# Kernel optimization log

Measured on AMD Instinct MI355X. Metric: run time of the kernel, lower is better.

The kernel has to match this reference:

```python
import jax, jax.numpy as jnp
import numpy as np

LN_EPS = 1e-5  # torch.nn.LayerNorm default

def g(x):
    # minGRU activation: x + 0.5 for x >= 0, sigmoid(x) otherwise (always positive)
    return jnp.where(x >= 0, x + 0.5, jax.nn.sigmoid(x))

def log_g(x):
    return jnp.where(x >= 0, jnp.log(jax.nn.relu(x) + 0.5), -jax.nn.softplus(-x))

def layernorm(x, gamma, beta):
    mu = jnp.mean(x, axis=-1, keepdims=True)
    var = jnp.var(x, axis=-1, keepdims=True)
    return (x - mu) * jax.lax.rsqrt(var + LN_EPS) * gamma + beta

def mingru_scan(gate, hidden, h0):
    # gate, hidden: (B,S,D); h0: (B,1,D) positive
    # z = sigmoid(gate); h_t = (1-z_t)*h_{t-1} + z_t * g(hidden_t)
    # evaluated via Heinsen parallel scan in log space
    log_z = -jax.nn.softplus(-gate)          # log sigmoid(gate)
    log_coeffs = -jax.nn.softplus(gate)      # log(1 - sigmoid(gate))
    log_h0 = jnp.log(h0)                     # (B,1,D)
    log_tilde_h = log_g(hidden)
    a_star = jnp.cumsum(
        jnp.concatenate([jnp.zeros_like(log_h0), log_coeffs], axis=1), axis=1
    )                                        # (B,S+1,D)
    log_vals = jnp.concatenate([log_h0, log_z + log_tilde_h], axis=1) - a_star
    log_h = a_star + jax.lax.cumlogsumexp(log_vals, axis=1)
    return jnp.exp(log_h)[:, 1:]             # (B,S,D)

def setup_inputs() -> dict:
    key = jax.random.key(0)
    k1, k2 = jax.random.split(key)
    B, S, D, L = 8, 4096, 1024, 3
    x = jax.random.normal(k1, (B, S, D), dtype=jnp.float32)
    W = jax.random.normal(k2, (L, D, 2 * D), dtype=jnp.float32) * 0.02
    b = jnp.zeros((L, 2 * D), dtype=jnp.float32)
    ln_gamma = jnp.ones((L, D), dtype=jnp.float32)
    ln_beta = jnp.zeros((L, D), dtype=jnp.float32)
    return {"x": x, "ln_gamma": ln_gamma, "ln_beta": ln_beta, "W": W, "b": b}

def reference(x, ln_gamma, ln_beta, W, b):
    B, S, D = x.shape
    L = W.shape[0]
    inp = x
    next_hidden = []
    for l in range(L):
        h_prev = jnp.full((B, 1, D), 0.5, dtype=x.dtype)  # g(zeros) = 0.5
        xn = layernorm(inp, ln_gamma[l], ln_beta[l])
        gh = jnp.einsum('bsd,de->bse', xn, W[l]) + b[l]   # (B,S,2D)
        gate, hidden = jnp.split(gh, 2, axis=2)
        out = mingru_scan(gate, hidden, h_prev)
        next_hidden.append(out[:, -1:])
        out = out + inp  # residual (sizes equal -> identity res_align)
        inp = out
    return (out, *next_hidden)
```

## Files before the change

kernel.cpp:

```cpp
#include <hip/hip_runtime.h>

typedef unsigned short u16;
typedef unsigned int   u32;
typedef float  f32x2  __attribute__((ext_vector_type(2)));
typedef float  f32x4  __attribute__((ext_vector_type(4)));
typedef short  bf16x8 __attribute__((ext_vector_type(8)));
typedef u16    u16x4  __attribute__((ext_vector_type(4)));
typedef u32    u32x4  __attribute__((ext_vector_type(4)));

#define BQ 8
#define SQ 4096
#define DQ 1024
#define NQ 2048
#define MQ 32768
#define KQ 1024
#define CCH 128
#define TCH 32
#define NT 16

__device__ __forceinline__ float bf2f(u16 u){
  union { u32 i; float f; } v; v.i = ((u32)u) << 16; return v.f;
}
__device__ __forceinline__ u16 f2bf(float f){
  union { float f; u32 i; } v; v.f = f;
  u32 r = v.i + 0x7fffu + ((v.i >> 16) & 1u);
  return (u16)(r >> 16);
}

__device__ __forceinline__ void sig_ab(float gate, float hid, float& a, float& bv){
  float eg = __expf(gate);
  float a_ = __builtin_amdgcn_rcpf(1.f + eg);
  float z  = 1.f - a_;
  float eh = __expf(hid);
  float sg = eh * __builtin_amdgcn_rcpf(1.f + eh);
  float gval = (hid >= 0.f) ? (hid + 0.5f) : sg;
  a = a_; bv = z * gval;
}

__device__ __forceinline__ void gload_lds16(const u16* g, u16* l){
  __builtin_amdgcn_global_load_lds(
      (const __attribute__((address_space(1))) u32*)g,
      (__attribute__((address_space(3)))       u32*)l,
      16, 0, 0);
}

__global__ __launch_bounds__(256) void wt_cast(const float* __restrict__ W,
                                               u16* __restrict__ WT){
  __shared__ float t[64][65];
  const int l  = blockIdx.z;
  const int k0 = blockIdx.x << 6, n0 = blockIdx.y << 6;
  const float* Wl = W  + (size_t)l * KQ * NQ;
  u16*         Tl = WT + (size_t)l * NQ * KQ;
  const int c = threadIdx.x & 63, r4 = threadIdx.x >> 6;
  #pragma unroll
  for (int i = 0; i < 16; ++i){
    int r = i * 4 + r4;
    t[r][c] = Wl[(size_t)(k0 + r) * NQ + n0 + c];
  }
  __syncthreads();
  #pragma unroll
  for (int i = 0; i < 16; ++i){
    int r = i * 4 + r4;
    Tl[(size_t)(n0 + r) * KQ + k0 + c] = f2bf(t[c][r]);
  }
}

__global__ __launch_bounds__(256) void ln_cast(const float* __restrict__ x,
                                               const float* __restrict__ gamma,
                                               const float* __restrict__ beta,
                                               u16* __restrict__ xn){
  const size_t row = blockIdx.x;
  const int tid = threadIdx.x;
  f32x4 xv = *(const f32x4*)(x + row * DQ + tid * 4);
  float s  = xv[0] + xv[1] + xv[2] + xv[3];
  float s2 = xv[0]*xv[0] + xv[1]*xv[1] + xv[2]*xv[2] + xv[3]*xv[3];
  #pragma unroll
  for (int off = 32; off > 0; off >>= 1){
    s  += __shfl_down(s,  off);
    s2 += __shfl_down(s2, off);
  }
  __shared__ float red[8];
  const int wave = tid >> 6, lane = tid & 63;
  if (lane == 0){ red[wave] = s; red[4 + wave] = s2; }
  __syncthreads();
  s  = red[0] + red[1] + red[2] + red[3];
  s2 = red[4] + red[5] + red[6] + red[7];
  const float mean = s * (1.f / DQ);
  float var = fmaxf(s2 * (1.f / DQ) - mean * mean, 0.f);
  const float rstd = rsqrtf(var + 1e-5f);
  f32x4 gv = *(const f32x4*)(gamma + tid * 4);
  f32x4 bv = *(const f32x4*)(beta  + tid * 4);
  u16x4 o;
  #pragma unroll
  for (int e = 0; e < 4; ++e) o[e] = f2bf((xv[e] - mean) * rstd * gv[e] + bv[e]);
  *(u16x4*)(xn + row * DQ + tid * 4) = o;
}

__global__ __launch_bounds__(512, 2) void gemm_k8(const u16* __restrict__ A,
                                                  const u16* __restrict__ Bt,
                                                  const float* __restrict__ bias,
                                                  u32* __restrict__ abv,
                                                  float* __restrict__ pq){
  __shared__ u16 lds[2][2][2][8192];
  const int bid = blockIdx.x;
  const int swz = ((bid & 7) << 7) | (bid >> 3);
  const int bn = swz & 7, bm = swz >> 3;
  const int m0 = bm << 8;
  const int tid = threadIdx.x;
  const int w = tid >> 6, lane = tid & 63;
  const int wr = w >> 2, wc = w & 3;
  const int lr = lane & 15, hi = lane >> 4;
  const int sl8 = lane >> 3;
  const int sslot = (lane & 7) ^ sl8;

  f32x4 acc[2][2][4][2] = {};
  bf16x8 afrA[4][2], afrB[4][2];
  bf16x8 bf0[2][2], bf1[2][2];

#define FENCE asm volatile("" ::: "memory")
#define BAR do { FENCE; __builtin_amdgcn_s_barrier(); FENCE; } while(0)

#define STAGE(op, hf, kt, pb_) do {                                            \
    const u16* gsrc_ = (op) ? Bt : A;                                          \
    const int rb_ = (op) ? ((bn << 7) + (hf) * 1024) : (m0 + ((hf) << 7));     \
    _Pragma("unroll")                                                          \
    for (int g_ = 0; g_ < 2; ++g_){                                            \
      const int row_ = (w << 4) + (g_ << 3) + sl8;                             \
      gload_lds16(gsrc_ + (size_t)(rb_ + row_) * KQ + ((kt) << 6) + (sslot << 3),\
                  &lds[pb_][op][hf][((w << 4) + (g_ << 3)) << 6]);             \
    }                                                                          \
  } while(0)

#define LDSRD(dst, base_, row_, slot_) do {                                    \
    const int r_ = (row_);                                                     \
    dst = *(const bf16x8*)((const char*)(base_) +                              \
          ((r_ << 7) + ((((slot_)) ^ (r_ & 7)) << 4)));                        \
  } while(0)

#define RD_A(dst, hf, buf_) do {                                               \
    const u16* Ah_ = &lds[buf_][0][hf][0];                                     \
    _Pragma("unroll")                                                          \
    for (int i_ = 0; i_ < 4; ++i_)                                             \
      _Pragma("unroll")                                                        \
      for (int kk_ = 0; kk_ < 2; ++kk_)                                        \
        LDSRD(dst[i_][kk_], Ah_, (wr << 6) + (i_ << 4) + lr, (kk_ << 2) + hi); \
  } while(0)

#define RD_B(dst, hf, buf_) do {                                               \
    const u16* Bh_ = &lds[buf_][1][hf][0];                                     \
    _Pragma("unroll")                                                          \
    for (int j_ = 0; j_ < 2; ++j_)                                             \
      _Pragma("unroll")                                                        \
      for (int kk_ = 0; kk_ < 2; ++kk_)                                        \
        LDSRD(dst[j_][kk_], Bh_, (wc << 5) + (j_ << 4) + lr, (kk_ << 2) + hi); \
  } while(0)

#define MM(qm, qn, AR, B) do {                                                 \
    _Pragma("unroll")                                                          \
    for (int kk_ = 0; kk_ < 2; ++kk_)                                          \
      _Pragma("unroll")                                                        \
      for (int i_ = 0; i_ < 4; ++i_)                                           \
        _Pragma("unroll")                                                      \
        for (int j_ = 0; j_ < 2; ++j_)                                         \
          acc[qm][qn][i_][j_] = __builtin_amdgcn_mfma_f32_16x16x32_bf16(       \
              AR[i_][kk_], B[j_][kk_], acc[qm][qn][i_][j_], 0, 0, 0);          \
  } while(0)

  STAGE(0, 0, 0, 0); STAGE(1, 0, 0, 0); STAGE(0, 1, 0, 0); STAGE(1, 1, 0, 0);

  for (int t = 0; t < NT; ++t){
    const int pb = t & 1, qb = pb ^ 1;
    const bool s = (t + 1 < NT);
    asm volatile("s_waitcnt vmcnt(0)" ::: "memory");
    BAR;
    if (s){
      STAGE(0, 0, t + 1, qb); STAGE(1, 0, t + 1, qb);
      STAGE(0, 1, t + 1, qb); STAGE(1, 1, t + 1, qb);
    }
    RD_A(afrA, 0, pb); RD_B(bf0, 0, pb);
    RD_A(afrB, 1, pb); RD_B(bf1, 1, pb);
    __builtin_amdgcn_s_setprio(1);
    MM(0, 0, afrA, bf0);
    MM(0, 1, afrA, bf1);
    MM(1, 0, afrB, bf0);
    MM(1, 1, afrB, bf1);
    __builtin_amdgcn_s_setprio(0);
  }
#undef MM
#undef RD_B
#undef RD_A
#undef LDSRD
#undef STAGE

  const int dbase = (bn << 7) + (wc << 5) + lr;
  #pragma unroll
  for (int qm = 0; qm < 2; ++qm){
    const int row00 = m0 + (qm << 7) + (wr << 6);
    #pragma unroll
    for (int half = 0; half < 2; ++half){
      float chP[2] = {1.f, 1.f}, chQ[2] = {0.f, 0.f};
      #pragma unroll
      for (int ii = 0; ii < 2; ++ii){
        const int i = (half << 1) + ii;
        float sgP[2] = {1.f, 1.f}, sgQ[2] = {0.f, 0.f};
        #pragma unroll
        for (int r = 0; r < 4; ++r){
          const int row = row00 + (i << 4) + (hi << 2) + r;
          #pragma unroll
          for (int j = 0; j < 2; ++j){
            const int d = dbase + (j << 4);
            float gate = acc[qm][0][i][j][r] + bias[d];
            float hid  = acc[qm][1][i][j][r] + bias[1024 + d];
            float a, bv; sig_ab(gate, hid, a, bv);
            u32 pk;
            asm volatile("v_cvt_pk_bf16_f32 %0, %1, %2"
                         : "=v"(pk) : "v"(a), "v"(bv));
            abv[(size_t)row * 1024 + d] = pk;
            union { u32 u; float f; } ua, ub;
            ua.u = pk << 16; ub.u = pk & 0xffff0000u;
            sgQ[j] = ua.f * sgQ[j] + ub.f;
            sgP[j] *= ua.f;
          }
        }
        #pragma unroll
        for (int j = 0; j < 2; ++j){
          float p = sgP[j], q = sgQ[j];
          float p1 = __shfl_up(p, 16), q1 = __shfl_up(q, 16);
          if (hi >= 1){ q = p * q1 + q; p = p * p1; }
          float p2 = __shfl_up(p, 32), q2 = __shfl_up(q, 32);
          if (hi >= 2){ q = p * q2 + q; p = p * p2; }
          chQ[j] = p * chQ[j] + q;
          chP[j] = p * chP[j];
        }
      }
      if (hi == 3){
        const int rowb = row00 + (half << 5);
        const int bq = rowb >> 12, cq = (rowb >> 5) & (CCH - 1);
        #pragma unroll
        for (int j = 0; j < 2; ++j){
          const int d = dbase + (j << 4);
          f32x2 v; v[0] = chP[j]; v[1] = chQ[j];
          *(f32x2*)(pq + ((((size_t)(bq * CCH + cq)) << 10) + d) * 2) = v;
        }
      }
    }
  }
#undef BAR
#undef FENCE
}

__global__ __launch_bounds__(256) void scan2(const float* __restrict__ pq,
                                             float* __restrict__ hst,
                                             float* __restrict__ hlast){
  const int idx = blockIdx.x * 256 + threadIdx.x;
  const int b = idx >> 10, d = idx & 1023;
  float h = 0.5f;
  for (int c = 0; c < CCH; ++c){
    const size_t o = ((size_t)(b * CCH + c) << 10) + d;
    hst[o] = h;
    f32x2 v = *(const f32x2*)(pq + o * 2);
    h = v[0] * h + v[1];
  }
  hlast[idx] = h;
}

template<int MODE>
__global__ __launch_bounds__(256) void scan3f(const u32* __restrict__ abv,
                                              const float* __restrict__ hst,
                                              const void* __restrict__ inp,
                                              void* __restrict__ outp,
                                              u16* __restrict__ xn,
                                              const float* __restrict__ gamma,
                                              const float* __restrict__ beta){
  const int b = blockIdx.x >> 7;
  const int c = blockIdx.x & (CCH - 1);
  const int tid = threadIdx.x;
  const int d4 = tid << 2;
  const int wave = tid >> 6, lane = tid & 63;
  const size_t srow = (size_t)b * SQ + (size_t)c * TCH;
  const u32* base = abv + srow * 1024 + d4;
  const size_t o = ((size_t)blockIdx.x << 10) + d4;
  f32x4 h0v = *(const f32x4*)(hst + o);
  float h[4] = {h0v[0], h0v[1], h0v[2], h0v[3]};
  __shared__ float red[2][8];
  f32x4 gv = {}, bvv = {};
  if (MODE != 2){
    gv  = *(const f32x4*)(gamma + d4);
    bvv = *(const f32x4*)(beta  + d4);
  }
  for (int t = 0; t < TCH; ++t){
    u32x4 ab = *(const u32x4*)(base + (size_t)t * 1024);
    f32x4 iv;
    if (MODE == 0){
      iv = *(const f32x4*)((const float*)inp + (srow + t) * DQ + d4);
    } else {
      u16x4 ib = *(const u16x4*)((const u16*)inp + (srow + t) * DQ + d4);
      #pragma unroll
      for (int e = 0; e < 4; ++e) iv[e] = bf2f(ib[e]);
    }
    f32x4 ov;
    #pragma unroll
    for (int e = 0; e < 4; ++e){
      const float a  = bf2f((u16)(ab[e] & 0xffffu));
      const float bv = bf2f((u16)(ab[e] >> 16));
      h[e] = a * h[e] + bv;
      ov[e] = h[e] + iv[e];
    }
    if (MODE == 2){
      *(f32x4*)((float*)outp + (srow + t) * DQ + d4) = ov;
    } else {
      u16x4 ob;
      #pragma unroll
      for (int e = 0; e < 4; ++e) ob[e] = f2bf(ov[e]);
      *(u16x4*)((u16*)outp + (srow + t) * DQ + d4) = ob;
      float s  = ov[0] + ov[1] + ov[2] + ov[3];
      float s2 = ov[0]*ov[0] + ov[1]*ov[1] + ov[2]*ov[2] + ov[3]*ov[3];
      #pragma unroll
      for (int off = 32; off > 0; off >>= 1){
        s  += __shfl_down(s,  off);
        s2 += __shfl_down(s2, off);
      }
      const int rb = t & 1;
      if (lane == 0){ red[rb][wave] = s; red[rb][4 + wave] = s2; }
      __syncthreads();
      s  = red[rb][0] + red[rb][1] + red[rb][2] + red[rb][3];
      s2 = red[rb][4] + red[rb][5] + red[rb][6] + red[rb][7];
      const float mean = s * (1.f / DQ);
      float var = fmaxf(s2 * (1.f / DQ) - mean * mean, 0.f);
      const float rstd = rsqrtf(var + 1e-5f);
      u16x4 xo;
      #pragma unroll
      for (int e = 0; e < 4; ++e)
        xo[e] = f2bf((ov[e] - mean) * rstd * gv[e] + bvv[e]);
      *(u16x4*)(xn + (srow + t) * DQ + d4) = xo;
    }
  }
}

extern "C" void kernel_launch(void* const* d_in, const int* in_sizes, int n_in,
                              void* d_out, int out_size, void* d_ws, size_t ws_size,
                              hipStream_t stream) {
  const float* x     = (const float*)d_in[0];
  const float* gamma = (const float*)d_in[1];
  const float* beta  = (const float*)d_in[2];
  const float* W     = (const float*)d_in[3];
  const float* bias  = (const float*)d_in[4];
  float* out = (float*)d_out;

  char* ws = (char*)d_ws;
  const size_t ACT = (size_t)MQ * DQ * 4;
  u16*   bufA = (u16*)(ws);
  u16*   bufB = (u16*)(ws + ACT);
  u32*   abv  = (u32*)(ws + 2 * ACT);
  u16*   xn   = (u16*)(ws + 3 * ACT);
  u16*   WT   = (u16*)(ws + 3 * ACT + (size_t)MQ * DQ * 2);
  float* pq   = (float*)(ws + 3 * ACT + (size_t)MQ * DQ * 2 + (size_t)3 * NQ * KQ * 2);
  float* hst  = pq + (size_t)2 * BQ * CCH * DQ;

  wt_cast<<<dim3(KQ / 64, NQ / 64, 3), 256, 0, stream>>>(W, WT);

  const dim3 ggrid((NQ / 256) * (MQ / 256));
  ln_cast<<<MQ, 256, 0, stream>>>(x, gamma, beta, xn);
  gemm_k8<<<ggrid, 512, 0, stream>>>(xn, WT, bias, abv, pq);
  scan2<<<(BQ * DQ) / 256, 256, 0, stream>>>(pq, hst, out + (size_t)MQ * DQ);
  scan3f<0><<<BQ * CCH, 256, 0, stream>>>(abv, hst, x, bufA, xn,
                                          gamma + DQ, beta + DQ);
  gemm_k8<<<ggrid, 512, 0, stream>>>(xn, WT + (size_t)NQ * KQ, bias + NQ,
                                     abv, pq);
  scan2<<<(BQ * DQ) / 256, 256, 0, stream>>>(pq, hst,
                                             out + (size_t)MQ * DQ + BQ * DQ);
  scan3f<1><<<BQ * CCH, 256, 0, stream>>>(abv, hst, bufA, bufB, xn,
                                          gamma + 2 * DQ, beta + 2 * DQ);
  gemm_k8<<<ggrid, 512, 0, stream>>>(xn, WT + (size_t)2 * NQ * KQ, bias + 2 * NQ,
                                     abv, pq);
  scan2<<<(BQ * DQ) / 256, 256, 0, stream>>>(pq, hst,
                                             out + (size_t)MQ * DQ + 2 * BQ * DQ);
  scan3f<2><<<BQ * CCH, 256, 0, stream>>>(abv, hst, bufB, out, nullptr,
                                          nullptr, nullptr);
}
```

Baseline: 720.5 us.

## Load GEMM B operand directly from global into registers, bypassing LDS

The B (weight) tile is no longer staged through shared memory. Each wave now reads its own B fragments straight from global memory into registers every k-step, while only A stays double-buffered in LDS. This halves LDS usage and removes the B LDS writes and reads. In exchange, the B loads are issued and consumed in the same iteration, so their global latency is not hidden behind the previous step. Waves in different rows also fetch the same B data redundantly.

```diff
diff --git a/kernel.cpp b/kernel.cpp
--- a/kernel.cpp
+++ b/kernel.cpp
@@ -101,7 +101,7 @@
                                                   const float* __restrict__ bias,
                                                   u32* __restrict__ abv,
                                                   float* __restrict__ pq){
-  __shared__ u16 lds[2][2][2][8192];
+  __shared__ u16 lds[2][2][8192];
   const int bid = blockIdx.x;
   const int swz = ((bid & 7) << 7) | (bid >> 3);
   const int bn = swz & 7, bm = swz >> 3;
@@ -112,23 +112,37 @@
   const int lr = lane & 15, hi = lane >> 4;
   const int sl8 = lane >> 3;
   const int sslot = (lane & 7) ^ sl8;
+  const int brow = (bn << 7) + (wc << 5) + lr;
 
   f32x4 acc[2][2][4][2] = {};
   bf16x8 afrA[4][2], afrB[4][2];
-  bf16x8 bf0[2][2], bf1[2][2];
+  bf16x8 bgl[2][2][2];
 
 #define FENCE asm volatile("" ::: "memory")
 #define BAR do { FENCE; __builtin_amdgcn_s_barrier(); FENCE; } while(0)
 
-#define STAGE(op, hf, kt, pb_) do {                                            \
-    const u16* gsrc_ = (op) ? Bt : A;                                          \
-    const int rb_ = (op) ? ((bn << 7) + (hf) * 1024) : (m0 + ((hf) << 7));     \
+#define STAGE_A(kt, pb_) do {                                                  \
     _Pragma("unroll")                                                          \
-    for (int g_ = 0; g_ < 2; ++g_){                                            \
-      const int row_ = (w << 4) + (g_ << 3) + sl8;                             \
-      gload_lds16(gsrc_ + (size_t)(rb_ + row_) * KQ + ((kt) << 6) + (sslot << 3),\
-                  &lds[pb_][op][hf][((w << 4) + (g_ << 3)) << 6]);             \
-    }                                                                          \
+    for (int hf_ = 0; hf_ < 2; ++hf_)                                          \
+      _Pragma("unroll")                                                        \
+      for (int g_ = 0; g_ < 2; ++g_){                                          \
+        const int row_ = (w << 4) + (g_ << 3) + sl8;                           \
+        gload_lds16(A + (size_t)(m0 + (hf_ << 7) + row_) * KQ + ((kt) << 6) +  \
+                        (sslot << 3),                                          \
+                    &lds[pb_][hf_][((w << 4) + (g_ << 3)) << 6]);              \
+      }                                                                        \
+  } while(0)
+
+#define LD_B(kt) do {                                                          \
+    _Pragma("unroll")                                                          \
+    for (int qn_ = 0; qn_ < 2; ++qn_)                                          \
+      _Pragma("unroll")                                                        \
+      for (int j_ = 0; j_ < 2; ++j_)                                           \
+        _Pragma("unroll")                                                      \
+        for (int kk_ = 0; kk_ < 2; ++kk_)                                      \
+          bgl[qn_][j_][kk_] = *(const bf16x8*)(Bt +                            \
+              ((size_t)(brow + qn_ * 1024 + (j_ << 4)) << 10) +                \
+              ((kt) << 6) + (kk_ << 5) + (hi << 3));                           \
   } while(0)
 
 #define LDSRD(dst, base_, row_, slot_) do {                                    \
@@ -138,7 +152,7 @@
   } while(0)
 
 #define RD_A(dst, hf, buf_) do {                                               \
-    const u16* Ah_ = &lds[buf_][0][hf][0];                                     \
+    const u16* Ah_ = &lds[buf_][hf][0];                                        \
     _Pragma("unroll")                                                          \
     for (int i_ = 0; i_ < 4; ++i_)                                             \
       _Pragma("unroll")                                                        \
@@ -146,16 +160,7 @@
         LDSRD(dst[i_][kk_], Ah_, (wr << 6) + (i_ << 4) + lr, (kk_ << 2) + hi); \
   } while(0)
 
-#define RD_B(dst, hf, buf_) do {                                               \
-    const u16* Bh_ = &lds[buf_][1][hf][0];                                     \
-    _Pragma("unroll")                                                          \
-    for (int j_ = 0; j_ < 2; ++j_)                                             \
-      _Pragma("unroll")                                                        \
-      for (int kk_ = 0; kk_ < 2; ++kk_)                                        \
-        LDSRD(dst[j_][kk_], Bh_, (wc << 5) + (j_ << 4) + lr, (kk_ << 2) + hi); \
-  } while(0)
-
-#define MM(qm, qn, AR, B) do {                                                 \
+#define MM(qm, qn, AR) do {                                                    \
     _Pragma("unroll")                                                          \
     for (int kk_ = 0; kk_ < 2; ++kk_)                                          \
       _Pragma("unroll")                                                        \
@@ -163,34 +168,31 @@
         _Pragma("unroll")                                                      \
         for (int j_ = 0; j_ < 2; ++j_)                                         \
           acc[qm][qn][i_][j_] = __builtin_amdgcn_mfma_f32_16x16x32_bf16(       \
-              AR[i_][kk_], B[j_][kk_], acc[qm][qn][i_][j_], 0, 0, 0);          \
-  } while(0)
-
-  STAGE(0, 0, 0, 0); STAGE(1, 0, 0, 0); STAGE(0, 1, 0, 0); STAGE(1, 1, 0, 0);
+              AR[i_][kk_], bgl[qn][j_][kk_], acc[qm][qn][i_][j_], 0, 0, 0);    \
+  } while(0)
+
+  STAGE_A(0, 0);
 
   for (int t = 0; t < NT; ++t){
     const int pb = t & 1, qb = pb ^ 1;
     const bool s = (t + 1 < NT);
     asm volatile("s_waitcnt vmcnt(0)" ::: "memory");
     BAR;
-    if (s){
-      STAGE(0, 0, t + 1, qb); STAGE(1, 0, t + 1, qb);
-      STAGE(0, 1, t + 1, qb); STAGE(1, 1, t + 1, qb);
-    }
-    RD_A(afrA, 0, pb); RD_B(bf0, 0, pb);
-    RD_A(afrB, 1, pb); RD_B(bf1, 1, pb);
+    if (s) STAGE_A(t + 1, qb);
+    LD_B(t);
+    RD_A(afrA, 0, pb); RD_A(afrB, 1, pb);
     __builtin_amdgcn_s_setprio(1);
-    MM(0, 0, afrA, bf0);
-    MM(0, 1, afrA, bf1);
-    MM(1, 0, afrB, bf0);
-    MM(1, 1, afrB, bf1);
+    MM(0, 0, afrA);
+    MM(0, 1, afrA);
+    MM(1, 0, afrB);
+    MM(1, 1, afrB);
     __builtin_amdgcn_s_setprio(0);
   }
 #undef MM
-#undef RD_B
 #undef RD_A
 #undef LDSRD
-#undef STAGE
+#undef LD_B
+#undef STAGE_A
 
   const int dbase = (bn << 7) + (wc << 5) + lr;
   #pragma unroll
```

New measurement: 936.5 us. 1.3x slower.
